# Kernel tuning notes

Measured on AMD Instinct MI355X. Metric: run time of the kernel, lower is better.

Reference implementation:

```python
import jax, jax.numpy as jnp
import numpy as np

N_HEAD = 16
D_HEAD = 64
SCALE = 1.0 / D_HEAD ** 0.5


def setup_inputs() -> dict:
    key = jax.random.key(0)
    k1, k2, k3, k4 = jax.random.split(key, 4)
    bsz, qlen, d_embed, d_model = 4, 1024, 768, 1024
    return {
        "word_emb": jax.random.normal(k1, (bsz, qlen, d_embed), dtype=jnp.float32),
        "emb_w": jax.random.normal(k2, (d_embed, d_model), dtype=jnp.float32) * 0.02,
        "emb_b": jnp.zeros((d_model,), dtype=jnp.float32),
        "qkv_w0": jax.random.normal(k3, (d_model, 3 * N_HEAD * D_HEAD), dtype=jnp.float32) * 0.02,
        "qkv_w1": jax.random.normal(k4, (d_model, 3 * N_HEAD * D_HEAD), dtype=jnp.float32) * 0.02,
    }


def _mha(h, qkv_w):
    # h: [qlen, bsz, d_model]
    qlen, bsz, _ = h.shape
    heads = h @ qkv_w  # [qlen, bsz, 3*n_head*d_head]
    head_q, head_k, head_v = jnp.split(heads, 3, axis=-1)
    head_q = head_q.reshape(qlen, bsz, N_HEAD, D_HEAD)
    head_k = head_k.reshape(qlen, bsz, N_HEAD, D_HEAD)
    head_v = head_v.reshape(qlen, bsz, N_HEAD, D_HEAD)
    # explicit score materialization, faithful to the source einsum pattern
    attn_score = jnp.einsum('ibnd,jbnd->ijbn', head_q, head_k) * SCALE
    attn_prob = jax.nn.softmax(attn_score, axis=1)  # softmax over klen (dim=1)
    attn_vec = jnp.einsum('ijbn,jbnd->ibnd', attn_prob, head_v)
    attn_vec = attn_vec.reshape(qlen, bsz, N_HEAD * D_HEAD)
    return attn_vec, attn_prob


def reference(word_emb, emb_w, emb_b, qkv_w0, qkv_w1):
    # word_emb: [bsz, qlen, d_embed] -> [qlen, bsz, d_embed]
    h = jnp.transpose(word_emb, (1, 0, 2))
    h = h @ emb_w + emb_b  # emb_proj since d_embed != d_model
    # NOTE: the source computes pos_emb and word_emb + pos_emb, but then
    # overwrites with core_out = self.drop(word_emb), discarding pos_emb.
    # Dropout is identity in reference (eval) mode, so core_out == h.
    core_out = h
    core_out, attn_maps = _mha(core_out, qkv_w0)
    core_out, attn_maps = _mha(core_out, qkv_w1)
    return core_out, attn_maps
```

## Files before the change

kernel.cpp:

```cpp
#include <hip/hip_runtime.h>

#define LOG2E 1.44269504088896340736f

typedef __attribute__((ext_vector_type(8))) short short8;
typedef __attribute__((ext_vector_type(4))) short short4v;
typedef __attribute__((ext_vector_type(4))) float floatx4;

__device__ __forceinline__ float bf2f(short s) {
    union { float f; unsigned u; } v; v.u = ((unsigned)(unsigned short)s) << 16; return v.f;
}
__device__ __forceinline__ short f2bf(float f) {
    union { float f; unsigned u; } v; v.f = f;
    unsigned u = v.u;
    u += 0x7FFFu + ((u >> 16) & 1u);
    return (short)(u >> 16);
}

__device__ __forceinline__ void gl_lds16(const void* g, void* l) {
    __builtin_amdgcn_global_load_lds((const __attribute__((address_space(1))) void*)g,
                                     (__attribute__((address_space(3))) void*)l, 16, 0, 0);
}

__device__ __forceinline__ void wcast_tile(const float* __restrict__ W,
                                           short* __restrict__ Wt, int K, int N,
                                           int n0, int k0, int t) {
    __shared__ float tile[64][65];
    int r = t >> 2, c4 = (t & 3) * 16;
    const float* src = W + (size_t)(k0 + r) * N + n0 + c4;
#pragma unroll
    for (int q = 0; q < 16; ++q) tile[r][c4 + q] = src[q];
    __syncthreads();
    short* dst = Wt + (size_t)(n0 + r) * K + k0 + c4;
    short8 o1, o2;
#pragma unroll
    for (int q = 0; q < 8; ++q) o1[q] = f2bf(tile[c4 + q][r]);
#pragma unroll
    for (int q = 0; q < 8; ++q) o2[q] = f2bf(tile[c4 + 8 + q][r]);
    *(short8*)(dst) = o1;
    *(short8*)(dst + 8) = o2;
}

__global__ __launch_bounds__(256) void prep(const float* __restrict__ we,
                                            const float* __restrict__ emb_w,
                                            const float* __restrict__ qkv_w0,
                                            const float* __restrict__ qkv_w1,
                                            short* __restrict__ A0,
                                            short* __restrict__ WtE,
                                            short* __restrict__ Wt0,
                                            short* __restrict__ Wt1) {
    int bid = blockIdx.x, t = threadIdx.x;
    if (bid < 1536) {
        int e = bid * 256 + t;
        int m = e / 96, dc = (e % 96) * 8;
        int b = m & 3, s = m >> 2;
        const float* src = we + (size_t)(b * 1024 + s) * 768 + dc;
        short8 o;
#pragma unroll
        for (int q = 0; q < 8; ++q) o[q] = f2bf(src[q]);
        *(short8*)(A0 + (size_t)m * 768 + dc) = o;
    } else if (bid < 1728) {
        int tt = bid - 1536;
        wcast_tile(emb_w, WtE, 768, 1024, (tt & 15) * 64, (tt >> 4) * 64, t);
    } else if (bid < 2496) {
        int tt = bid - 1728;
        wcast_tile(qkv_w0, Wt0, 1024, 3072, (tt % 48) * 64, (tt / 48) * 64, t);
    } else {
        int tt = bid - 2496;
        wcast_tile(qkv_w1, Wt1, 1024, 3072, (tt % 48) * 64, (tt / 48) * 64, t);
    }
}

__global__ __launch_bounds__(256) void gemm_bt(const short* __restrict__ A,
                                               const short* __restrict__ Bt,
                                               short* __restrict__ C,
                                               const float* __restrict__ bias,
                                               int K, int N) {
    __shared__ __align__(16) short sA[128 * 64];
    __shared__ __align__(16) short sB[128 * 64];
    int n0 = blockIdx.x * 128, m0 = blockIdx.y * 128;
    int tid = threadIdx.x;
    int lane = tid & 63, w = tid >> 6;
    int wm = (w >> 1) * 64, wn = (w & 1) * 64;
    int l15 = lane & 15, quad = lane >> 4;
    int lrow = lane >> 3, lchunk = (lane & 7) ^ lrow;

    floatx4 zero = {0.f, 0.f, 0.f, 0.f};
    floatx4 acc[4][4];
#pragma unroll
    for (int i = 0; i < 4; ++i)
#pragma unroll
        for (int j = 0; j < 4; ++j) acc[i][j] = zero;

    for (int k0 = 0; k0 < K; k0 += 64) {
#pragma unroll
        for (int c = 0; c < 4; ++c) {
            int r0 = w * 32 + c * 8;
            int row = r0 + lrow;
            gl_lds16(A + (size_t)(m0 + row) * K + k0 + lchunk * 8, sA + r0 * 64);
            gl_lds16(Bt + (size_t)(n0 + row) * K + k0 + lchunk * 8, sB + r0 * 64);
        }
        __syncthreads();
#pragma unroll
        for (int h = 0; h < 2; ++h) {
            int sw = ((h * 4 + quad) ^ (l15 & 7)) * 8;
            short8 af[4], bfr[4];
#pragma unroll
            for (int i = 0; i < 4; ++i) {
                af[i]  = *(const short8*)(sA + (wm + i * 16 + l15) * 64 + sw);
                bfr[i] = *(const short8*)(sB + (wn + i * 16 + l15) * 64 + sw);
            }
#pragma unroll
            for (int i = 0; i < 4; ++i)
#pragma unroll
                for (int j = 0; j < 4; ++j)
                    acc[i][j] = __builtin_amdgcn_mfma_f32_16x16x32_bf16(bfr[j], af[i], acc[i][j], 0, 0, 0);
        }
        __syncthreads();
    }
#pragma unroll
    for (int i = 0; i < 4; ++i) {
        int row = m0 + wm + i * 16 + l15;
#pragma unroll
        for (int j = 0; j < 4; ++j) {
            int colb = n0 + wn + j * 16 + quad * 4;
            float4 bv = bias ? *(const float4*)(bias + colb) : float4{0.f, 0.f, 0.f, 0.f};
            short4v st;
            st[0] = f2bf(acc[i][j][0] + bv.x);
            st[1] = f2bf(acc[i][j][1] + bv.y);
            st[2] = f2bf(acc[i][j][2] + bv.z);
            st[3] = f2bf(acc[i][j][3] + bv.w);
            *(short4v*)(C + (size_t)row * N + colb) = st;
        }
    }
}

__global__ __launch_bounds__(256) void pack_qkv(const short* __restrict__ heads,
                                                short* __restrict__ Qp,
                                                short* __restrict__ Kp,
                                                short* __restrict__ Vtp) {
    __shared__ short vt[64][72];
    int bn = blockIdx.y;
    int b = bn >> 4, n = bn & 15;
    int j0 = blockIdx.x * 64;
    int t = threadIdx.x;
#pragma unroll
    for (int h = 0; h < 2; ++h) {
        int c = t + h * 256;
        int jj = c >> 3, off = (c & 7) * 8;
        const short* base = heads + (size_t)((j0 + jj) * 4 + b) * 3072 + n * 64 + off;
        short8 qv = *(const short8*)(base);
        short8 kv = *(const short8*)(base + 1024);
        short8 vv = *(const short8*)(base + 2048);
        short8 qs;
#pragma unroll
        for (int e = 0; e < 8; ++e) qs[e] = f2bf(bf2f(qv[e]) * 0.125f);
        *(short8*)(Qp + (size_t)bn * 65536 + (j0 + jj) * 64 + off) = qs;
        *(short8*)(Kp + (size_t)bn * 65536 + (j0 + jj) * 64 + off) = kv;
#pragma unroll
        for (int e = 0; e < 8; ++e) vt[jj][off + e] = vv[e];
    }
    __syncthreads();
#pragma unroll
    for (int h = 0; h < 2; ++h) {
        int c = t + h * 256;
        int d = c >> 3, joff = (c & 7) * 8;
        short8 o;
#pragma unroll
        for (int e = 0; e < 8; ++e) o[e] = vt[joff + e][d];
        *(short8*)(Vtp + (size_t)bn * 65536 + d * 1024 + j0 + joff) = o;
    }
}

template <bool L2>
__global__ __launch_bounds__(64) void fattn(const short* __restrict__ Qp,
                                            const short* __restrict__ Kp,
                                            const short* __restrict__ Vtp,
                                            void* __restrict__ Optr,
                                            float* __restrict__ linv) {
    __shared__ __align__(16) short plds[32 * 32];
    int bn = blockIdx.y, b = bn >> 4, n = bn & 15;
    int i0 = blockIdx.x * 32;
    int lane = threadIdx.x, l15 = lane & 15, quad = lane >> 4;
    const short* Qb = Qp + (size_t)bn * 65536;
    const short* Kb = Kp + (size_t)bn * 65536;
    const short* Vb = Vtp + (size_t)bn * 65536;

    short8 qf[2][2];
#pragma unroll
    for (int ib = 0; ib < 2; ++ib) {
        qf[ib][0] = *(const short8*)(Qb + (i0 + ib * 16 + l15) * 64 + quad * 8);
        qf[ib][1] = *(const short8*)(Qb + (i0 + ib * 16 + l15) * 64 + 32 + quad * 8);
    }
    floatx4 zero = {0.f, 0.f, 0.f, 0.f};
    floatx4 o[2][4];
#pragma unroll
    for (int ib = 0; ib < 2; ++ib)
#pragma unroll
        for (int tt = 0; tt < 4; ++tt) o[ib][tt] = zero;
    float lsum[2] = {0.f, 0.f};

    for (int j0 = 0; j0 < 1024; j0 += 32) {
#pragma unroll
        for (int jb = 0; jb < 2; ++jb) {
            const short* kr = Kb + (j0 + jb * 16 + l15) * 64 + quad * 8;
            short8 kf0 = *(const short8*)(kr);
            short8 kf1 = *(const short8*)(kr + 32);
#pragma unroll
            for (int ib = 0; ib < 2; ++ib) {
                floatx4 s = zero;
                s = __builtin_amdgcn_mfma_f32_16x16x32_bf16(kf0, qf[ib][0], s, 0, 0, 0);
                s = __builtin_amdgcn_mfma_f32_16x16x32_bf16(kf1, qf[ib][1], s, 0, 0, 0);
                short4v pk;
                float ls = 0.f;
#pragma unroll
                for (int r = 0; r < 4; ++r) {
                    float p = __builtin_amdgcn_exp2f(s[r] * LOG2E);
                    ls += p;
                    pk[r] = f2bf(p);
                }
                lsum[ib] += ls;
                *(short4v*)(plds + (ib * 16 + l15) * 32 + jb * 16 + quad * 4) = pk;
            }
        }
        __syncthreads();
        short8 pa[2];
        pa[0] = *(const short8*)(plds + l15 * 32 + quad * 8);
        pa[1] = *(const short8*)(plds + (16 + l15) * 32 + quad * 8);
#pragma unroll
        for (int tt = 0; tt < 4; ++tt) {
            short8 vf = *(const short8*)(Vb + (tt * 16 + l15) * 1024 + j0 + quad * 8);
#pragma unroll
            for (int ib = 0; ib < 2; ++ib)
                o[ib][tt] = __builtin_amdgcn_mfma_f32_16x16x32_bf16(vf, pa[ib], o[ib][tt], 0, 0, 0);
        }
        __syncthreads();
    }
    float rinv[2];
#pragma unroll
    for (int ib = 0; ib < 2; ++ib) {
        float t = lsum[ib];
        t += __shfl_xor(t, 16);
        t += __shfl_xor(t, 32);
        rinv[ib] = 1.f / t;
    }
    if (L2 && quad == 0) {
        linv[bn * 1024 + i0 + l15] = rinv[0];
        linv[bn * 1024 + i0 + 16 + l15] = rinv[1];
    }
#pragma unroll
    for (int ib = 0; ib < 2; ++ib)
#pragma unroll
        for (int tt = 0; tt < 4; ++tt) {
            int row = i0 + ib * 16 + l15;
            int colb = n * 64 + tt * 16 + quad * 4;
            size_t idx = (size_t)(row * 4 + b) * 1024 + colb;
            if (L2) {
                float4 v;
                v.x = o[ib][tt][0] * rinv[ib];
                v.y = o[ib][tt][1] * rinv[ib];
                v.z = o[ib][tt][2] * rinv[ib];
                v.w = o[ib][tt][3] * rinv[ib];
                *(float4*)((float*)Optr + idx) = v;
            } else {
                short4v st;
#pragma unroll
                for (int r = 0; r < 4; ++r) st[r] = f2bf(o[ib][tt][r] * rinv[ib]);
                *(short4v*)((short*)Optr + idx) = st;
            }
        }
}

__global__ __launch_bounds__(256) void pfin(const short* __restrict__ Qp,
                                            const short* __restrict__ Kp,
                                            const float* __restrict__ linv,
                                            float* __restrict__ Pout) {
    __shared__ short sP[64 * 512];
    int j0 = blockIdx.x * 32, i0 = blockIdx.y * 16;
    int tid = threadIdx.x, wv = tid >> 6, lane = tid & 63;
    int l15 = lane & 15, quad = lane >> 4;
    floatx4 zero = {0.f, 0.f, 0.f, 0.f};
    for (int bi = 0; bi < 16; ++bi) {
        int bn = wv * 16 + bi;
        const short* Qb = Qp + (size_t)bn * 65536;
        const short* Kb = Kp + (size_t)bn * 65536;
        short8 qf0 = *(const short8*)(Qb + (i0 + l15) * 64 + quad * 8);
        short8 qf1 = *(const short8*)(Qb + (i0 + l15) * 64 + 32 + quad * 8);
        float li = linv[bn * 1024 + i0 + l15];
#pragma unroll
        for (int jb = 0; jb < 2; ++jb) {
            const short* kr = Kb + (j0 + jb * 16 + l15) * 64 + quad * 8;
            short8 kf0 = *(const short8*)(kr);
            short8 kf1 = *(const short8*)(kr + 32);
            floatx4 s = zero;
            s = __builtin_amdgcn_mfma_f32_16x16x32_bf16(kf0, qf0, s, 0, 0, 0);
            s = __builtin_amdgcn_mfma_f32_16x16x32_bf16(kf1, qf1, s, 0, 0, 0);
            short4v pk;
#pragma unroll
            for (int r = 0; r < 4; ++r)
                pk[r] = f2bf(__builtin_amdgcn_exp2f(s[r] * LOG2E) * li);
            *(short4v*)(sP + bn * 512 + l15 * 32 + jb * 16 + quad * 4) = pk;
        }
    }
    __syncthreads();
    int ii = tid >> 4, q = tid & 15;
    float* dst = Pout + (size_t)(i0 + ii) * 65536 + j0 * 64 + q * 128;
#pragma unroll
    for (int e4 = 0; e4 < 32; ++e4) {
        int pos = q * 128 + e4 * 4;
        int jj = pos >> 6, bnb = pos & 63;
        float4 v;
        v.x = bf2f(sP[(bnb + 0) * 512 + ii * 32 + jj]);
        v.y = bf2f(sP[(bnb + 1) * 512 + ii * 32 + jj]);
        v.z = bf2f(sP[(bnb + 2) * 512 + ii * 32 + jj]);
        v.w = bf2f(sP[(bnb + 3) * 512 + ii * 32 + jj]);
        *(float4*)(dst + e4 * 4) = v;
    }
}

extern "C" void kernel_launch(void* const* d_in, const int* in_sizes, int n_in,
                              void* d_out, int out_size, void* d_ws, size_t ws_size,
                              hipStream_t stream) {
    const float* word_emb = (const float*)d_in[0];
    const float* emb_w    = (const float*)d_in[1];
    const float* emb_b    = (const float*)d_in[2];
    const float* qkv_w0   = (const float*)d_in[3];
    const float* qkv_w1   = (const float*)d_in[4];
    float* out0 = (float*)d_out;
    float* out1 = out0 + 4194304;

    char* ws = (char*)d_ws;
    short* A0    = (short*)(ws);
    short* WtE   = (short*)(ws + 6291456);
    short* Wt0   = (short*)(ws + 7864320);
    short* Wt1   = (short*)(ws + 14155776);
    short* hbuf  = (short*)(ws + 20447232);
    short* h2    = (short*)(ws + 28835840);
    short* heads = (short*)(ws + 37224448);
    short* Qp    = (short*)(ws + 62390272);
    short* Kp    = (short*)(ws + 70778880);
    short* Vtp   = (short*)(ws + 79167488);
    float* linv  = (float*)(ws + 87556096);

    prep<<<3264, 256, 0, stream>>>(word_emb, emb_w, qkv_w0, qkv_w1, A0, WtE, Wt0, Wt1);

    gemm_bt<<<dim3(8, 32), 256, 0, stream>>>(A0, WtE, hbuf, emb_b, 768, 1024);
    gemm_bt<<<dim3(24, 32), 256, 0, stream>>>(hbuf, Wt0, heads, nullptr, 1024, 3072);
    pack_qkv<<<dim3(16, 64), 256, 0, stream>>>(heads, Qp, Kp, Vtp);
    fattn<false><<<dim3(32, 64), 64, 0, stream>>>(Qp, Kp, Vtp, (void*)h2, nullptr);
    gemm_bt<<<dim3(24, 32), 256, 0, stream>>>(h2, Wt1, heads, nullptr, 1024, 3072);
    pack_qkv<<<dim3(16, 64), 256, 0, stream>>>(heads, Qp, Kp, Vtp);
    fattn<true><<<dim3(32, 64), 64, 0, stream>>>(Qp, Kp, Vtp, (void*)out0, linv);
    pfin<<<dim3(32, 64), 256, 0, stream>>>(Qp, Kp, linv, out1);
}
```

Before: 666.3 us.

## Fuse QKV packing into GEMM epilogue and cache unnormalized probabilities for output

The QKV GEMM epilogue now scatters Q (pre-scaled), K and V directly into per-head layouts, removing the heads buffer round trip; a smaller pack_v kernel only transposes V. The second attention pass writes unnormalized bf16 probabilities to a workspace so pfin just rescales and transposes them instead of recomputing QK^T and exp. Attention blocks are remapped so each XCD handles a contiguous set of heads for L2 locality. This trades recompute for an extra bf16 write and read of the probability tensor, and uses scattered short4 stores in the GEMM epilogue.

```diff
diff --git a/kernel.cpp b/kernel.cpp
--- a/kernel.cpp
+++ b/kernel.cpp
@@ -70,11 +70,15 @@
     }
 }
 
+template <int PACK>
 __global__ __launch_bounds__(256) void gemm_bt(const short* __restrict__ A,
                                                const short* __restrict__ Bt,
                                                short* __restrict__ C,
                                                const float* __restrict__ bias,
-                                               int K, int N) {
+                                               int K, int N,
+                                               short* __restrict__ Qp,
+                                               short* __restrict__ Kp,
+                                               short* __restrict__ Vp) {
     __shared__ __align__(16) short sA[128 * 64];
     __shared__ __align__(16) short sB[128 * 64];
     int n0 = blockIdx.x * 128, m0 = blockIdx.y * 128;
@@ -123,41 +127,42 @@
 #pragma unroll
         for (int j = 0; j < 4; ++j) {
             int colb = n0 + wn + j * 16 + quad * 4;
-            float4 bv = bias ? *(const float4*)(bias + colb) : float4{0.f, 0.f, 0.f, 0.f};
-            short4v st;
-            st[0] = f2bf(acc[i][j][0] + bv.x);
-            st[1] = f2bf(acc[i][j][1] + bv.y);
-            st[2] = f2bf(acc[i][j][2] + bv.z);
-            st[3] = f2bf(acc[i][j][3] + bv.w);
-            *(short4v*)(C + (size_t)row * N + colb) = st;
-        }
-    }
-}
-
-__global__ __launch_bounds__(256) void pack_qkv(const short* __restrict__ heads,
-                                                short* __restrict__ Qp,
-                                                short* __restrict__ Kp,
-                                                short* __restrict__ Vtp) {
+            if (PACK == 0) {
+                float4 bv = bias ? *(const float4*)(bias + colb) : float4{0.f, 0.f, 0.f, 0.f};
+                short4v st;
+                st[0] = f2bf(acc[i][j][0] + bv.x);
+                st[1] = f2bf(acc[i][j][1] + bv.y);
+                st[2] = f2bf(acc[i][j][2] + bv.z);
+                st[3] = f2bf(acc[i][j][3] + bv.w);
+                *(short4v*)(C + (size_t)row * N + colb) = st;
+            } else {
+                int sel = colb >> 10, nn = colb & 1023;
+                int bn = ((row & 3) << 4) + (nn >> 6);
+                size_t idx = (size_t)bn * 65536 + (size_t)(row >> 2) * 64 + (nn & 63);
+                float sc = (sel == 0) ? 0.125f : 1.0f;
+                short4v st;
+#pragma unroll
+                for (int r = 0; r < 4; ++r) st[r] = f2bf(acc[i][j][r] * sc);
+                short* dst = (sel == 0) ? Qp : (sel == 1 ? Kp : Vp);
+                *(short4v*)(dst + idx) = st;
+            }
+        }
+    }
+}
+
+__global__ __launch_bounds__(256) void pack_v(const short* __restrict__ Vp,
+                                              short* __restrict__ Vtp) {
     __shared__ short vt[64][72];
     int bn = blockIdx.y;
-    int b = bn >> 4, n = bn & 15;
-    int j0 = blockIdx.x * 64;
+    int t0 = blockIdx.x * 64;
     int t = threadIdx.x;
 #pragma unroll
     for (int h = 0; h < 2; ++h) {
         int c = t + h * 256;
-        int jj = c >> 3, off = (c & 7) * 8;
-        const short* base = heads + (size_t)((j0 + jj) * 4 + b) * 3072 + n * 64 + off;
-        short8 qv = *(const short8*)(base);
-        short8 kv = *(const short8*)(base + 1024);
-        short8 vv = *(const short8*)(base + 2048);
-        short8 qs;
-#pragma unroll
-        for (int e = 0; e < 8; ++e) qs[e] = f2bf(bf2f(qv[e]) * 0.125f);
-        *(short8*)(Qp + (size_t)bn * 65536 + (j0 + jj) * 64 + off) = qs;
-        *(short8*)(Kp + (size_t)bn * 65536 + (j0 + jj) * 64 + off) = kv;
-#pragma unroll
-        for (int e = 0; e < 8; ++e) vt[jj][off + e] = vv[e];
+        int tt = c >> 3, off = (c & 7) * 8;
+        short8 v = *(const short8*)(Vp + (size_t)bn * 65536 + (size_t)(t0 + tt) * 64 + off);
+#pragma unroll
+        for (int e = 0; e < 8; ++e) vt[tt][off + e] = v[e];
     }
     __syncthreads();
 #pragma unroll
@@ -167,7 +172,7 @@
         short8 o;
 #pragma unroll
         for (int e = 0; e < 8; ++e) o[e] = vt[joff + e][d];
-        *(short8*)(Vtp + (size_t)bn * 65536 + d * 1024 + j0 + joff) = o;
+        *(short8*)(Vtp + (size_t)bn * 65536 + (size_t)d * 1024 + t0 + joff) = o;
     }
 }
 
@@ -176,10 +181,14 @@
                                             const short* __restrict__ Kp,
                                             const short* __restrict__ Vtp,
                                             void* __restrict__ Optr,
-                                            float* __restrict__ linv) {
+                                            float* __restrict__ linv,
+                                            short* __restrict__ Pp) {
     __shared__ __align__(16) short plds[32 * 32];
-    int bn = blockIdx.y, b = bn >> 4, n = bn & 15;
-    int i0 = blockIdx.x * 32;
+    int bid = blockIdx.x;
+    int xcd = bid & 7, wid = bid >> 3;
+    int bn = xcd * 8 + (wid >> 5);
+    int i0 = (wid & 31) * 32;
+    int b = bn >> 4, n = bn & 15;
     int lane = threadIdx.x, l15 = lane & 15, quad = lane >> 4;
     const short* Qb = Qp + (size_t)bn * 65536;
     const short* Kb = Kp + (size_t)bn * 65536;
@@ -220,6 +229,10 @@
                 }
                 lsum[ib] += ls;
                 *(short4v*)(plds + (ib * 16 + l15) * 32 + jb * 16 + quad * 4) = pk;
+                if (L2) {
+                    *(short4v*)(Pp + (size_t)bn * 1048576 +
+                                (size_t)(i0 + ib * 16 + l15) * 1024 + j0 + jb * 16 + quad * 4) = pk;
+                }
             }
         }
         __syncthreads();
@@ -270,39 +283,26 @@
         }
 }
 
-__global__ __launch_bounds__(256) void pfin(const short* __restrict__ Qp,
-                                            const short* __restrict__ Kp,
+__global__ __launch_bounds__(256) void pfin(const short* __restrict__ Pp,
                                             const float* __restrict__ linv,
                                             float* __restrict__ Pout) {
     __shared__ short sP[64 * 512];
     int j0 = blockIdx.x * 32, i0 = blockIdx.y * 16;
-    int tid = threadIdx.x, wv = tid >> 6, lane = tid & 63;
-    int l15 = lane & 15, quad = lane >> 4;
-    floatx4 zero = {0.f, 0.f, 0.f, 0.f};
-    for (int bi = 0; bi < 16; ++bi) {
-        int bn = wv * 16 + bi;
-        const short* Qb = Qp + (size_t)bn * 65536;
-        const short* Kb = Kp + (size_t)bn * 65536;
-        short8 qf0 = *(const short8*)(Qb + (i0 + l15) * 64 + quad * 8);
-        short8 qf1 = *(const short8*)(Qb + (i0 + l15) * 64 + 32 + quad * 8);
-        float li = linv[bn * 1024 + i0 + l15];
-#pragma unroll
-        for (int jb = 0; jb < 2; ++jb) {
-            const short* kr = Kb + (j0 + jb * 16 + l15) * 64 + quad * 8;
-            short8 kf0 = *(const short8*)(kr);
-            short8 kf1 = *(const short8*)(kr + 32);
-            floatx4 s = zero;
-            s = __builtin_amdgcn_mfma_f32_16x16x32_bf16(kf0, qf0, s, 0, 0, 0);
-            s = __builtin_amdgcn_mfma_f32_16x16x32_bf16(kf1, qf1, s, 0, 0, 0);
-            short4v pk;
-#pragma unroll
-            for (int r = 0; r < 4; ++r)
-                pk[r] = f2bf(__builtin_amdgcn_exp2f(s[r] * LOG2E) * li);
-            *(short4v*)(sP + bn * 512 + l15 * 32 + jb * 16 + quad * 4) = pk;
-        }
+    int t = threadIdx.x;
+#pragma unroll
+    for (int h = 0; h < 16; ++h) {
+        int c = t + h * 256;
+        int bn = c >> 6, rem = c & 63, ii = rem >> 2, part = rem & 3;
+        short8 v = *(const short8*)(Pp + (size_t)bn * 1048576 +
+                                    (size_t)(i0 + ii) * 1024 + j0 + part * 8);
+        float li = linv[bn * 1024 + i0 + ii];
+        short8 sv;
+#pragma unroll
+        for (int e = 0; e < 8; ++e) sv[e] = f2bf(bf2f(v[e]) * li);
+        *(short8*)(sP + bn * 512 + ii * 32 + part * 8) = sv;
     }
     __syncthreads();
-    int ii = tid >> 4, q = tid & 15;
+    int ii = t >> 4, q = t & 15;
     float* dst = Pout + (size_t)(i0 + ii) * 65536 + j0 * 64 + q * 128;
 #pragma unroll
     for (int e4 = 0; e4 < 32; ++e4) {
@@ -335,20 +335,24 @@
     short* Wt1   = (short*)(ws + 14155776);
     short* hbuf  = (short*)(ws + 20447232);
     short* h2    = (short*)(ws + 28835840);
-    short* heads = (short*)(ws + 37224448);
-    short* Qp    = (short*)(ws + 62390272);
-    short* Kp    = (short*)(ws + 70778880);
-    short* Vtp   = (short*)(ws + 79167488);
-    float* linv  = (float*)(ws + 87556096);
+    short* Qp    = (short*)(ws + 37224448);
+    short* Kp    = (short*)(ws + 45613056);
+    short* Vp    = (short*)(ws + 54001664);
+    short* Vtp   = (short*)(ws + 62390272);
+    float* linv  = (float*)(ws + 70778880);
+    short* Pp    = (short*)(ws + 71041024);
 
     prep<<<3264, 256, 0, stream>>>(word_emb, emb_w, qkv_w0, qkv_w1, A0, WtE, Wt0, Wt1);
 
-    gemm_bt<<<dim3(8, 32), 256, 0, stream>>>(A0, WtE, hbuf, emb_b, 768, 1024);
-    gemm_bt<<<dim3(24, 32), 256, 0, stream>>>(hbuf, Wt0, heads, nullptr, 1024, 3072);
-    pack_qkv<<<dim3(16, 64), 256, 0, stream>>>(heads, Qp, Kp, Vtp);
-    fattn<false><<<dim3(32, 64), 64, 0, stream>>>(Qp, Kp, Vtp, (void*)h2, nullptr);
-    gemm_bt<<<dim3(24, 32), 256, 0, stream>>>(h2, Wt1, heads, nullptr, 1024, 3072);
-    pack_qkv<<<dim3(16, 64), 256, 0, stream>>>(heads, Qp, Kp, Vtp);
-    fattn<true><<<dim3(32, 64), 64, 0, stream>>>(Qp, Kp, Vtp, (void*)out0, linv);
-    pfin<<<dim3(32, 64), 256, 0, stream>>>(Qp, Kp, linv, out1);
-}
+    gemm_bt<0><<<dim3(8, 32), 256, 0, stream>>>(A0, WtE, hbuf, emb_b, 768, 1024,
+                                                nullptr, nullptr, nullptr);
+    gemm_bt<1><<<dim3(24, 32), 256, 0, stream>>>(hbuf, Wt0, nullptr, nullptr, 1024, 3072,
+                                                 Qp, Kp, Vp);
+    pack_v<<<dim3(16, 64), 256, 0, stream>>>(Vp, Vtp);
+    fattn<false><<<2048, 64, 0, stream>>>(Qp, Kp, Vtp, (void*)h2, nullptr, nullptr);
+    gemm_bt<1><<<dim3(24, 32), 256, 0, stream>>>(h2, Wt1, nullptr, nullptr, 1024, 3072,
+                                                 Qp, Kp, Vp);
+    pack_v<<<dim3(16, 64), 256, 0, stream>>>(Vp, Vtp);
+    fattn<true><<<2048, 64, 0, stream>>>(Qp, Kp, Vtp, (void*)out0, linv, Pp);
+    pfin<<<dim3(32, 64), 256, 0, stream>>>(Pp, linv, out1);
+}
```

New measurement: 683.3 us. 2.6% more time.
